# Kernel optimization log

Hardware: AMD Instinct MI355X
Metric: run time of the kernel (lower is better)

Reference implementation:

```python
import jax, jax.numpy as jnp
import numpy as np


def lstm_cell(x, h, c, Wih, Whh, bih, bhh):
    # PyTorch LSTMCell: gates ordered (i, f, g, o)
    gates = x @ Wih.T + h @ Whh.T + bih + bhh
    i, f, g, o = jnp.split(gates, 4, axis=-1)
    c_new = jax.nn.sigmoid(f) * c + jax.nn.sigmoid(i) * jnp.tanh(g)
    h_new = jax.nn.sigmoid(o) * jnp.tanh(c_new)
    return h_new, c_new


def setup_inputs() -> dict:
    key = jax.random.key(0)
    B, S, I, H = 64, 1024, 300, 512
    ks = jax.random.split(key, 9)
    s0 = 1.0 / np.sqrt(H)  # PyTorch LSTMCell default init range

    def u(k, shape):
        return jax.random.uniform(k, shape, jnp.float32, -s0, s0)

    return {
        "input": jax.random.normal(ks[0], (B, S, I), jnp.float32),
        "Wih0": u(ks[1], (4 * H, I)),
        "Whh0": u(ks[2], (4 * H, H)),
        "bih0": u(ks[3], (4 * H,)),
        "bhh0": u(ks[4], (4 * H,)),
        "Wih1": u(ks[5], (4 * H, H)),
        "Whh1": u(ks[6], (4 * H, H)),
        "bih1": u(ks[7], (4 * H,)),
        "bhh1": u(ks[8], (4 * H,)),
    }


def reference(input, Wih0, Whh0, bih0, bhh0, Wih1, Whh1, bih1, bhh1):
    B, S, I = input.shape
    H = Whh0.shape[1]
    h0 = c0 = h1 = c1 = jnp.zeros((B, H), input.dtype)  # self.h0/self.c0 zeros

    def step(carry, x_t):
        h0, c0, h1, c1 = carry
        h0, c0 = lstm_cell(x_t, h0, c0, Wih0, Whh0, bih0, bhh0)
        h1, c1 = lstm_cell(h0, h1, c1, Wih1, Whh1, bih1, bhh1)
        return (h0, c0, h1, c1), (h1, c1)

    xs = jnp.swapaxes(input, 0, 1)  # [S, B, I]
    (h0, c0, h1, c1), (out, c_out) = jax.lax.scan(step, (h0, c0, h1, c1), xs)
    out = jnp.swapaxes(out, 0, 1)      # [B, S, H]
    c_out = jnp.swapaxes(c_out, 0, 1)  # [B, S, H]
    return ((out, c_out), (h1, c1))
```

## Files before the change

### kernel.cpp

```cpp
#include <hip/hip_runtime.h>

#define NB 64
#define NS 1024
#define NI 300
#define NH 512
#define NWG 224
#define L0N 64
#define L1N 128

typedef _Float16 f16;
typedef f16 half8 __attribute__((ext_vector_type(8)));
typedef float floatx4 __attribute__((ext_vector_type(4)));
typedef unsigned long long u64;
typedef unsigned u32;

__device__ __attribute__((aligned(64))) f16   g_X[NS][NB][320];
__device__ __attribute__((aligned(64))) f16   g_H0[4][NB][NH];
__device__ __attribute__((aligned(64))) f16   g_H1[4][NB][NH];
__device__ __attribute__((aligned(64))) float g_C1[4][NB][NH];
__device__ u32 g_flags[NWG];

__device__ __forceinline__ float sigm(float x){ return 1.f/(1.f+__expf(-x)); }
__device__ __forceinline__ float tanh_(float x){ return 1.f - 2.f/(__expf(2.f*x)+1.f); }

__device__ __forceinline__ u32 ld_flag(int i){
  return __hip_atomic_load(&g_flags[i], __ATOMIC_RELAXED, __HIP_MEMORY_SCOPE_AGENT);
}
__device__ __forceinline__ void sig_flag(int i, u32 v){
  __hip_atomic_store(&g_flags[i], v, __ATOMIC_RELAXED, __HIP_MEMORY_SCOPE_AGENT);
}

#define STR_(x) #x
#define STR(x) STR_(x)
#define CLOAD16(dst, base, OFF) \
  asm volatile("global_load_dwordx4 %0, %1, off offset:" STR(OFF) " sc0 sc1" \
               : "=v"(dst) : "v"(base))
#define CLOAD8(dst, base) \
  asm volatile("global_load_dwordx2 %0, %1, off sc0 sc1" : "=v"(dst) : "v"(base))
#define CLOADF4(dst, base) \
  asm volatile("global_load_dwordx4 %0, %1, off sc0 sc1" : "=v"(dst) : "v"(base))
#define CSTORE16(base, val) \
  asm volatile("global_store_dwordx4 %0, %1, off sc0 sc1" :: "v"(base), "v"(val))
#define CSTORE8(base, val) \
  asm volatile("global_store_dwordx2 %0, %1, off sc0 sc1" :: "v"(base), "v"(val))
#define VWAIT(N) do { asm volatile("s_waitcnt vmcnt(" STR(N) ")" ::: "memory"); \
  __builtin_amdgcn_sched_barrier(0); } while(0)
#define MFMA(acc, a, b) acc = __builtin_amdgcn_mfma_f32_16x16x32_f16(a, b, acc, 0, 0, 0)

__global__ void __launch_bounds__(256, 1) lstm_persist(
    const float* __restrict__ xin,
    const float* __restrict__ Wih0, const float* __restrict__ Whh0,
    const float* __restrict__ bih0, const float* __restrict__ bhh0,
    const float* __restrict__ Wih1, const float* __restrict__ Whh1,
    const float* __restrict__ bih1, const float* __restrict__ bhh1,
    float* __restrict__ out)
{
  __shared__ f16   Wl[16 * 840];
  __shared__ f16   sh_h[4][16][8];
  __shared__ float sh_c[4][16][4];
  __shared__ char  lds_pad[84000];

  const int wg = blockIdx.x, tid = threadIdx.x;
  const int wv = tid >> 6, lane = tid & 63, r15 = lane & 15, g4 = lane >> 4;
  const int kb = g4 * 8;
  const u32 base = ld_flag(wg);
  if (__builtin_expect(base == 0xdeadbeefu, 0)) ((volatile char*)lds_pad)[tid] = 1;

  if (wg < L0N) {
    const int j0 = wg * 8;
    const int mrow = wv * 16 + r15;
    {
      const int b = tid >> 2, q = tid & 3;
      for (int r = 0; r < 16; ++r) {
        const int t = wg * 16 + r;
        const float* xr = xin + ((size_t)b * NS + t) * NI;
        u64* dst = (u64*)&g_X[t][b][0];
        #pragma unroll
        for (int e = 0; e < 20; ++e) {
          const int idx = q * 20 + e;
          u64 v = 0;
          if (idx < 75) {
            const float4 f = *(const float4*)(xr + (idx << 2));
            union { f16 h[4]; u64 u; } pk;
            pk.h[0]=(f16)f.x; pk.h[1]=(f16)f.y; pk.h[2]=(f16)f.z; pk.h[3]=(f16)f.w;
            v = pk.u;
          }
          dst[idx] = v;
        }
      }
    }
    if (tid < 64) { half8 z = {}; CSTORE16(&g_H0[3][tid][j0], z); }
    half8 w0[26];
    {
      const int gc = ((r15 >> 3) * NH) + j0 + (r15 & 7);
      #pragma unroll
      for (int ch = 0; ch < 26; ++ch) {
        union { f16 h[8]; half8 v; } pk;
        #pragma unroll
        for (int jj = 0; jj < 8; ++jj) {
          const int k = ch * 32 + kb + jj;
          const float v = (k < NI) ? Wih0[(size_t)gc * NI + k]
                         : (k < 320) ? 0.f : Whh0[(size_t)gc * NH + (k - 320)];
          pk.h[jj] = (f16)v;
        }
        w0[ch] = pk.v;
      }
    }
    for (int r = 0; r < 16; ++r) {
      const int gc = (2 + (r >> 3)) * NH + j0 + (r & 7);
      for (int k = tid; k < 832; k += 256) {
        const float v = (k < NI) ? Wih0[(size_t)gc * NI + k]
                       : (k < 320) ? 0.f : Whh0[(size_t)gc * NH + (k - 320)];
        Wl[r * 840 + k] = (f16)v;
      }
    }
    const int jb = j0 + (r15 & 7);
    const float bi = bih0[jb] + bhh0[jb];
    const float bf = bih0[NH + jb] + bhh0[NH + jb];
    const float bg = bih0[2*NH + jb] + bhh0[2*NH + jb];
    const float bo = bih0[3*NH + jb] + bhh0[3*NH + jb];
    VWAIT(0);
    __syncthreads();
    if (tid == 0) { __threadfence(); sig_flag(wg, base + 1); }

    {
      const u32 T0 = base + 1;
      if (tid < 64) {
        for (;;) {
          const u32 f0 = ld_flag(tid);
          if (__all((int)(f0 - T0) >= 0)) break;
          __builtin_amdgcn_s_sleep(1);
        }
      }
      __syncthreads();
    }

    half8 xa[10];
    #pragma unroll
    for (int ci = 0; ci < 10; ++ci)
      xa[ci] = *(const half8*)&g_X[0][mrow][ci * 32 + kb];

    float creg[2] = {0.f, 0.f};
    const int hi = (r15 >> 3) & 1;
    const f16* wl = &Wl[r15 * 840 + kb];

    for (int t = 0; t < NS; ++t) {
      if (t > 0) {
        const u32 T0 = base + 1 + (u32)t;
        const u32 T1 = (t >= 4) ? (base + (u32)(t - 2)) : base;
        if (tid < 64) {
          for (;;) {
            const u32 f0 = ld_flag(tid);
            const u32 fa = ld_flag(64 + tid);
            const u32 fb = ld_flag(128 + tid);
            const bool ok = ((int)(f0 - T0) >= 0) & ((int)(fa - T1) >= 0) & ((int)(fb - T1) >= 0);
            if (__all(ok)) break;
            __builtin_amdgcn_s_sleep(1);
          }
        }
        __syncthreads();
      }
      const f16* hp = &g_H0[(t + 3) & 3][mrow][kb];
      half8 ha[16];
      CLOAD16(ha[0],  hp, 0);   CLOAD16(ha[1],  hp, 64);
      CLOAD16(ha[2],  hp, 128); CLOAD16(ha[3],  hp, 192);
      CLOAD16(ha[4],  hp, 256); CLOAD16(ha[5],  hp, 320);
      CLOAD16(ha[6],  hp, 384); CLOAD16(ha[7],  hp, 448);
      CLOAD16(ha[8],  hp, 512); CLOAD16(ha[9],  hp, 576);
      CLOAD16(ha[10], hp, 640); CLOAD16(ha[11], hp, 704);
      CLOAD16(ha[12], hp, 768); CLOAD16(ha[13], hp, 832);
      CLOAD16(ha[14], hp, 896); CLOAD16(ha[15], hp, 960);

      floatx4 a0a = {0,0,0,0}, a0b = {0,0,0,0}, a1a = {0,0,0,0}, a1b = {0,0,0,0};
      #pragma unroll
      for (int ci = 0; ci < 10; ++ci) {
        const half8 wb = *(const half8*)(wl + ci * 32);
        if (ci & 1) { MFMA(a0b, xa[ci], w0[ci]); MFMA(a1b, xa[ci], wb); }
        else        { MFMA(a0a, xa[ci], w0[ci]); MFMA(a1a, xa[ci], wb); }
      }
      VWAIT(8);
      #pragma unroll
      for (int ci = 0; ci < 8; ++ci) {
        const half8 wb = *(const half8*)(wl + (10 + ci) * 32);
        if (ci & 1) { MFMA(a0b, ha[ci], w0[10 + ci]); MFMA(a1b, ha[ci], wb); }
        else        { MFMA(a0a, ha[ci], w0[10 + ci]); MFMA(a1a, ha[ci], wb); }
      }
      VWAIT(0);
      #pragma unroll
      for (int ci = 8; ci < 16; ++ci) {
        const half8 wb = *(const half8*)(wl + (10 + ci) * 32);
        if (ci & 1) { MFMA(a0b, ha[ci], w0[10 + ci]); MFMA(a1b, ha[ci], wb); }
        else        { MFMA(a0a, ha[ci], w0[10 + ci]); MFMA(a1a, ha[ci], wb); }
      }
      const floatx4 acc0 = a0a + a0b, acc1 = a1a + a1b;

      float f0v[4], f1v[4];
      #pragma unroll
      for (int r = 0; r < 4; ++r) {
        f0v[r] = __shfl_xor(acc0[r], 8, 64);
        f1v[r] = __shfl_xor(acc1[r], 8, 64);
      }
      #pragma unroll
      for (int p = 0; p < 2; ++p) {
        const float vi = (hi ? f0v[2+p] : (float)acc0[p]) + bi;
        const float vf = (hi ? (float)acc0[2+p] : f0v[p]) + bf;
        const float vg = (hi ? f1v[2+p] : (float)acc1[p]) + bg;
        const float vo = (hi ? (float)acc1[2+p] : f1v[p]) + bo;
        const float cn = sigm(vf) * creg[p] + sigm(vi) * tanh_(vg);
        const float hn = sigm(vo) * tanh_(cn);
        creg[p] = cn;
        sh_h[wv][g4 * 4 + hi * 2 + p][r15 & 7] = (f16)hn;
      }
      if (lane < 16) {
        const half8 hv = *(const half8*)&sh_h[wv][lane][0];
        CSTORE16(&g_H0[t & 3][wv * 16 + lane][j0], hv);
      }
      VWAIT(0);
      __syncthreads();
      if (tid == 0) sig_flag(wg, base + 2 + (u32)t);
      if (t + 1 < NS) {
        #pragma unroll
        for (int ci = 0; ci < 10; ++ci)
          xa[ci] = *(const half8*)&g_X[t + 1][mrow][ci * 32 + kb];
      }
    }

  } else if (wg < L0N + L1N) {
    const int j0 = (wg - L0N) * 4;
    const int mrow = wv * 16 + r15;
    if (tid < 64) {
      u64 z = 0;
      CSTORE8(&g_H1[3][tid][j0], z);
    }
    half8 w1[24];
    {
      const int gc = (r15 >> 2) * NH + j0 + (r15 & 3);
      #pragma unroll
      for (int ch = 0; ch < 24; ++ch) {
        union { f16 h[8]; half8 v; } pk;
        #pragma unroll
        for (int jj = 0; jj < 8; ++jj) {
          const int k = ch * 32 + kb + jj;
          const float v = (k < NH) ? Wih1[(size_t)gc * NH + k]
                                   : Whh1[(size_t)gc * NH + (k - NH)];
          pk.h[jj] = (f16)v;
        }
        w1[ch] = pk.v;
      }
    }
    for (int r = 0; r < 16; ++r) {
      const int gc = (r >> 2) * NH + j0 + (r & 3);
      for (int k = tid; k < 256; k += 256)
        Wl[r * 264 + k] = (f16)Whh1[(size_t)gc * NH + 256 + k];
    }
    const int jb = j0 + (r15 & 3);
    const float bi = bih1[jb] + bhh1[jb];
    const float bf = bih1[NH + jb] + bhh1[NH + jb];
    const float bg = bih1[2*NH + jb] + bhh1[2*NH + jb];
    const float bo = bih1[3*NH + jb] + bhh1[3*NH + jb];
    VWAIT(0);
    __syncthreads();
    if (tid == 0) { __threadfence(); sig_flag(wg, base + 1); }

    float creg[2] = {0.f, 0.f};
    const f16* wl1 = &Wl[r15 * 264 + kb];

    for (int t = 0; t < NS; ++t) {
      {
        const u32 T0 = base + 2 + (u32)t;
        const u32 T1 = base + 1 + (u32)t;
        const u32 T2 = (t >= 4) ? (base + (u32)(t - 2)) : base;
        if (tid < 64) {
          for (;;) {
            const u32 f0 = ld_flag(tid);
            const u32 fa = ld_flag(64 + tid);
            const u32 fb = ld_flag(128 + tid);
            const u32 fo = ld_flag(192 + (tid & 31));
            const bool ok = ((int)(f0 - T0) >= 0) & ((int)(fa - T1) >= 0) &
                            ((int)(fb - T1) >= 0) & ((int)(fo - T2) >= 0);
            if (__all(ok)) break;
            __builtin_amdgcn_s_sleep(1);
          }
        }
        __syncthreads();
      }
      const f16* b0p = &g_H0[t & 3][mrow][kb];
      const f16* b1p = &g_H1[(t + 3) & 3][mrow][kb];
      half8 la[8], lb[8], lc[8], ld[8];
      CLOAD16(la[0], b0p, 0);   CLOAD16(la[1], b0p, 64);
      CLOAD16(la[2], b0p, 128); CLOAD16(la[3], b0p, 192);
      CLOAD16(la[4], b0p, 256); CLOAD16(la[5], b0p, 320);
      CLOAD16(la[6], b0p, 384); CLOAD16(la[7], b0p, 448);
      CLOAD16(lb[0], b0p, 512); CLOAD16(lb[1], b0p, 576);
      CLOAD16(lb[2], b0p, 640); CLOAD16(lb[3], b0p, 704);
      CLOAD16(lb[4], b0p, 768); CLOAD16(lb[5], b0p, 832);
      CLOAD16(lb[6], b0p, 896); CLOAD16(lb[7], b0p, 960);
      floatx4 aA = {0,0,0,0}, aB = {0,0,0,0};
      VWAIT(8);
      CLOAD16(lc[0], b1p, 0);   CLOAD16(lc[1], b1p, 64);
      CLOAD16(lc[2], b1p, 128); CLOAD16(lc[3], b1p, 192);
      CLOAD16(lc[4], b1p, 256); CLOAD16(lc[5], b1p, 320);
      CLOAD16(lc[6], b1p, 384); CLOAD16(lc[7], b1p, 448);
      #pragma unroll
      for (int cc = 0; cc < 8; ++cc) {
        if (cc & 1) MFMA(aB, la[cc], w1[cc]); else MFMA(aA, la[cc], w1[cc]);
      }
      VWAIT(8);
      CLOAD16(ld[0], b1p, 512); CLOAD16(ld[1], b1p, 576);
      CLOAD16(ld[2], b1p, 640); CLOAD16(ld[3], b1p, 704);
      CLOAD16(ld[4], b1p, 768); CLOAD16(ld[5], b1p, 832);
      CLOAD16(ld[6], b1p, 896); CLOAD16(ld[7], b1p, 960);
      #pragma unroll
      for (int cc = 0; cc < 8; ++cc) {
        if (cc & 1) MFMA(aB, lb[cc], w1[8 + cc]); else MFMA(aA, lb[cc], w1[8 + cc]);
      }
      VWAIT(8);
      #pragma unroll
      for (int cc = 0; cc < 8; ++cc) {
        if (cc & 1) MFMA(aB, lc[cc], w1[16 + cc]); else MFMA(aA, lc[cc], w1[16 + cc]);
      }
      VWAIT(0);
      #pragma unroll
      for (int cc = 0; cc < 8; ++cc) {
        const half8 wb = *(const half8*)(wl1 + cc * 32);
        if (cc & 1) MFMA(aB, ld[cc], wb); else MFMA(aA, ld[cc], wb);
      }
      const floatx4 av = aA + aB;

      float t4[4], t8[4], t12[4];
      #pragma unroll
      for (int r = 0; r < 4; ++r) {
        t4[r]  = __shfl_xor(av[r], 4, 64);
        t8[r]  = __shfl_xor(av[r], 8, 64);
        t12[r] = __shfl_xor(av[r], 12, 64);
      }
      if (r15 < 8) {
        const int q1 = r15 >> 2;
        #pragma unroll
        for (int p = 0; p < 2; ++p) {
          const float vi = (q1 ? t4[2+p]  : (float)av[p]) + bi;
          const float vf = (q1 ? (float)av[2+p] : t4[p])  + bf;
          const float vg = (q1 ? t12[2+p] : t8[p])        + bg;
          const float vo = (q1 ? t8[2+p]  : t12[p])       + bo;
          const float cn = sigm(vf) * creg[p] + sigm(vi) * tanh_(vg);
          const float hn = sigm(vo) * tanh_(cn);
          creg[p] = cn;
          const int rw = g4 * 4 + 2 * q1 + p;
          sh_h[wv][rw][r15 & 3] = (f16)hn;
          sh_c[wv][rw][r15 & 3] = cn;
        }
      }
      if (lane < 16) {
        const u64 hv = *(const u64*)&sh_h[wv][lane][0];
        CSTORE8(&g_H1[t & 3][wv * 16 + lane][j0], hv);
        const floatx4 cv = *(const floatx4*)&sh_c[wv][lane][0];
        CSTORE16(&g_C1[t & 3][wv * 16 + lane][j0], cv);
      }
      VWAIT(0);
      __syncthreads();
      if (tid == 0) sig_flag(wg, base + 2 + (u32)t);
    }

  } else {
    const int row = (wg - 192) * 2 + (tid >> 7);
    const int q = tid & 127;
    __syncthreads();
    if (tid == 0) sig_flag(wg, base + 1);
    for (int t = 0; t < NS; ++t) {
      {
        const u32 T = base + 2 + (u32)t;
        if (tid < 64) {
          for (;;) {
            const u32 fa = ld_flag(64 + tid);
            const u32 fb = ld_flag(128 + tid);
            if (__all(((int)(fa - T) >= 0) & ((int)(fb - T) >= 0))) break;
            __builtin_amdgcn_s_sleep(1);
          }
        }
        __syncthreads();
      }
      u64 hv; floatx4 cv;
      CLOAD8(hv, &g_H1[t & 3][row][q * 4]);
      CLOADF4(cv, &g_C1[t & 3][row][q * 4]);
      VWAIT(0);
      union { u64 u; f16 h[4]; } U; U.u = hv;
      floatx4 hf = { (float)U.h[0], (float)U.h[1], (float)U.h[2], (float)U.h[3] };
      const size_t o1 = (size_t)row * NS * NH + (size_t)t * NH + q * 4;
      *(floatx4*)&out[o1] = hf;
      *(floatx4*)&out[(size_t)NB * NS * NH + o1] = cv;
      if (t == NS - 1) {
        const size_t o2 = (size_t)2 * NB * NS * NH + (size_t)row * NH + q * 4;
        *(floatx4*)&out[o2] = hf;
        *(floatx4*)&out[o2 + (size_t)NB * NH] = cv;
      }
      __syncthreads();
      if (tid == 0) sig_flag(wg, base + 2 + (u32)t);
    }
  }
}

extern "C" void kernel_launch(void* const* d_in, const int* in_sizes, int n_in,
                              void* d_out, int out_size, void* d_ws, size_t ws_size,
                              hipStream_t stream) {
  (void)in_sizes; (void)n_in; (void)d_ws; (void)ws_size; (void)out_size;
  lstm_persist<<<dim3(NWG), dim3(256), 0, stream>>>(
      (const float*)d_in[0],
      (const float*)d_in[1], (const float*)d_in[2],
      (const float*)d_in[3], (const float*)d_in[4],
      (const float*)d_in[5], (const float*)d_in[6],
      (const float*)d_in[7], (const float*)d_in[8],
      (float*)d_out);
}
```

Baseline: 8.661 ms.

## Replace per-workgroup flag polling with per-step atomic arrival counters and register weights

Cross-workgroup synchronisation moves from per-workgroup flag arrays, which a whole wavefront polled across 64 to 192 entries, to per-timestep atomic arrival counters that one thread polls. Counter targets are derived from the run count read at launch. The layer-0 and layer-1 weights that were held in LDS now stay entirely in registers, which removes LDS reads from the MFMA loops but raises VGPR pressure. The loads for the next step's inputs are issued without cache-bypass bits, and layer-1 issues all its loads before waiting on any of them. Contention on the atomic counters and register spills are the main risks.

New measurement: 11.20 ms. 29.3% more time.

```diff
diff --git a/kernel.cpp b/kernel.cpp
--- a/kernel.cpp
+++ b/kernel.cpp
@@ -18,22 +18,28 @@
 __device__ __attribute__((aligned(64))) f16   g_H0[4][NB][NH];
 __device__ __attribute__((aligned(64))) f16   g_H1[4][NB][NH];
 __device__ __attribute__((aligned(64))) float g_C1[4][NB][NH];
-__device__ u32 g_flags[NWG];
+__device__ u32 g_arr0[NS];
+__device__ u32 g_arr1[NS];
+__device__ u32 g_arrOut[NS];
+__device__ u32 g_arrInit;
 
 __device__ __forceinline__ float sigm(float x){ return 1.f/(1.f+__expf(-x)); }
 __device__ __forceinline__ float tanh_(float x){ return 1.f - 2.f/(__expf(2.f*x)+1.f); }
 
-__device__ __forceinline__ u32 ld_flag(int i){
-  return __hip_atomic_load(&g_flags[i], __ATOMIC_RELAXED, __HIP_MEMORY_SCOPE_AGENT);
+__device__ __forceinline__ u32 ldc(const u32* p){
+  return __hip_atomic_load(p, __ATOMIC_RELAXED, __HIP_MEMORY_SCOPE_AGENT);
 }
-__device__ __forceinline__ void sig_flag(int i, u32 v){
-  __hip_atomic_store(&g_flags[i], v, __ATOMIC_RELAXED, __HIP_MEMORY_SCOPE_AGENT);
+__device__ __forceinline__ void arrive(u32* p){
+  __hip_atomic_fetch_add(p, 1u, __ATOMIC_RELAXED, __HIP_MEMORY_SCOPE_AGENT);
 }
 
 #define STR_(x) #x
 #define STR(x) STR_(x)
 #define CLOAD16(dst, base, OFF) \
   asm volatile("global_load_dwordx4 %0, %1, off offset:" STR(OFF) " sc0 sc1" \
+               : "=v"(dst) : "v"(base))
+#define CLOADN16(dst, base, OFF) \
+  asm volatile("global_load_dwordx4 %0, %1, off offset:" STR(OFF) \
                : "=v"(dst) : "v"(base))
 #define CLOAD8(dst, base) \
   asm volatile("global_load_dwordx2 %0, %1, off sc0 sc1" : "=v"(dst) : "v"(base))
@@ -55,7 +61,6 @@
     const float* __restrict__ bih1, const float* __restrict__ bhh1,
     float* __restrict__ out)
 {
-  __shared__ f16   Wl[16 * 840];
   __shared__ f16   sh_h[4][16][8];
   __shared__ float sh_c[4][16][4];
   __shared__ char  lds_pad[84000];
@@ -63,8 +68,14 @@
   const int wg = blockIdx.x, tid = threadIdx.x;
   const int wv = tid >> 6, lane = tid & 63, r15 = lane & 15, g4 = lane >> 4;
   const int kb = g4 * 8;
-  const u32 base = ld_flag(wg);
-  if (__builtin_expect(base == 0xdeadbeefu, 0)) ((volatile char*)lds_pad)[tid] = 1;
+
+  const u32 R64 = ldc(&g_arr0[NS - 1]);
+  const u32 R = R64 >> 6;
+  const u32 T_init = (R + 1) * 224;
+  const u32 T_a0 = R64 + 64;
+  const u32 T_a1 = (R64 << 1) + 128;
+  const u32 T_out = (R + 1) * 32;
+  if (__builtin_expect(R64 == 0xdeadbeefu, 0)) ((volatile char*)lds_pad)[tid] = 1;
 
   if (wg < L0N) {
     const int j0 = wg * 8;
@@ -90,28 +101,22 @@
       }
     }
     if (tid < 64) { half8 z = {}; CSTORE16(&g_H0[3][tid][j0], z); }
-    half8 w0[26];
+    half8 w0[26], w1r[26];
     {
-      const int gc = ((r15 >> 3) * NH) + j0 + (r15 & 7);
+      const int gc0 = ((r15 >> 3) * NH) + j0 + (r15 & 7);
+      const int gc1 = ((2 + (r15 >> 3)) * NH) + j0 + (r15 & 7);
       #pragma unroll
       for (int ch = 0; ch < 26; ++ch) {
-        union { f16 h[8]; half8 v; } pk;
+        union { f16 h[8]; half8 v; } p0, p1;
         #pragma unroll
         for (int jj = 0; jj < 8; ++jj) {
           const int k = ch * 32 + kb + jj;
-          const float v = (k < NI) ? Wih0[(size_t)gc * NI + k]
-                         : (k < 320) ? 0.f : Whh0[(size_t)gc * NH + (k - 320)];
-          pk.h[jj] = (f16)v;
-        }
-        w0[ch] = pk.v;
-      }
-    }
-    for (int r = 0; r < 16; ++r) {
-      const int gc = (2 + (r >> 3)) * NH + j0 + (r & 7);
-      for (int k = tid; k < 832; k += 256) {
-        const float v = (k < NI) ? Wih0[(size_t)gc * NI + k]
-                       : (k < 320) ? 0.f : Whh0[(size_t)gc * NH + (k - 320)];
-        Wl[r * 840 + k] = (f16)v;
+          p0.h[jj] = (f16)((k < NI) ? Wih0[(size_t)gc0 * NI + k]
+                     : (k < 320) ? 0.f : Whh0[(size_t)gc0 * NH + (k - 320)]);
+          p1.h[jj] = (f16)((k < NI) ? Wih0[(size_t)gc1 * NI + k]
+                     : (k < 320) ? 0.f : Whh0[(size_t)gc1 * NH + (k - 320)]);
+        }
+        w0[ch] = p0.v; w1r[ch] = p1.v;
       }
     }
     const int jb = j0 + (r15 & 7);
@@ -121,42 +126,32 @@
     const float bo = bih0[3*NH + jb] + bhh0[3*NH + jb];
     VWAIT(0);
     __syncthreads();
-    if (tid == 0) { __threadfence(); sig_flag(wg, base + 1); }
-
+    if (tid == 0) { __threadfence(); arrive(&g_arrInit); }
+
+    if (tid == 0) {
+      while ((int)(ldc(&g_arrInit) - T_init) < 0) __builtin_amdgcn_s_sleep(2);
+    }
+    __syncthreads();
+
+    half8 xa[10];
     {
-      const u32 T0 = base + 1;
-      if (tid < 64) {
-        for (;;) {
-          const u32 f0 = ld_flag(tid);
-          if (__all((int)(f0 - T0) >= 0)) break;
-          __builtin_amdgcn_s_sleep(1);
-        }
-      }
-      __syncthreads();
-    }
-
-    half8 xa[10];
-    #pragma unroll
-    for (int ci = 0; ci < 10; ++ci)
-      xa[ci] = *(const half8*)&g_X[0][mrow][ci * 32 + kb];
+      const f16* xp = &g_X[0][mrow][kb];
+      CLOADN16(xa[0], xp, 0);   CLOADN16(xa[1], xp, 64);
+      CLOADN16(xa[2], xp, 128); CLOADN16(xa[3], xp, 192);
+      CLOADN16(xa[4], xp, 256); CLOADN16(xa[5], xp, 320);
+      CLOADN16(xa[6], xp, 384); CLOADN16(xa[7], xp, 448);
+      CLOADN16(xa[8], xp, 512); CLOADN16(xa[9], xp, 576);
+    }
 
     float creg[2] = {0.f, 0.f};
     const int hi = (r15 >> 3) & 1;
-    const f16* wl = &Wl[r15 * 840 + kb];
 
     for (int t = 0; t < NS; ++t) {
       if (t > 0) {
-        const u32 T0 = base + 1 + (u32)t;
-        const u32 T1 = (t >= 4) ? (base + (u32)(t - 2)) : base;
-        if (tid < 64) {
-          for (;;) {
-            const u32 f0 = ld_flag(tid);
-            const u32 fa = ld_flag(64 + tid);
-            const u32 fb = ld_flag(128 + tid);
-            const bool ok = ((int)(f0 - T0) >= 0) & ((int)(fa - T1) >= 0) & ((int)(fb - T1) >= 0);
-            if (__all(ok)) break;
-            __builtin_amdgcn_s_sleep(1);
-          }
+        if (tid == 0) {
+          while ((int)(ldc(&g_arr0[t - 1]) - T_a0) < 0) __builtin_amdgcn_s_sleep(2);
+          if (t >= 4)
+            while ((int)(ldc(&g_arr1[t - 4]) - T_a1) < 0) __builtin_amdgcn_s_sleep(2);
         }
         __syncthreads();
       }
@@ -172,25 +167,23 @@
       CLOAD16(ha[14], hp, 896); CLOAD16(ha[15], hp, 960);
 
       floatx4 a0a = {0,0,0,0}, a0b = {0,0,0,0}, a1a = {0,0,0,0}, a1b = {0,0,0,0};
+      VWAIT(16);
       #pragma unroll
       for (int ci = 0; ci < 10; ++ci) {
-        const half8 wb = *(const half8*)(wl + ci * 32);
-        if (ci & 1) { MFMA(a0b, xa[ci], w0[ci]); MFMA(a1b, xa[ci], wb); }
-        else        { MFMA(a0a, xa[ci], w0[ci]); MFMA(a1a, xa[ci], wb); }
+        if (ci & 1) { MFMA(a0b, xa[ci], w0[ci]); MFMA(a1b, xa[ci], w1r[ci]); }
+        else        { MFMA(a0a, xa[ci], w0[ci]); MFMA(a1a, xa[ci], w1r[ci]); }
       }
       VWAIT(8);
       #pragma unroll
       for (int ci = 0; ci < 8; ++ci) {
-        const half8 wb = *(const half8*)(wl + (10 + ci) * 32);
-        if (ci & 1) { MFMA(a0b, ha[ci], w0[10 + ci]); MFMA(a1b, ha[ci], wb); }
-        else        { MFMA(a0a, ha[ci], w0[10 + ci]); MFMA(a1a, ha[ci], wb); }
+        if (ci & 1) { MFMA(a0b, ha[ci], w0[10 + ci]); MFMA(a1b, ha[ci], w1r[10 + ci]); }
+        else        { MFMA(a0a, ha[ci], w0[10 + ci]); MFMA(a1a, ha[ci], w1r[10 + ci]); }
       }
       VWAIT(0);
       #pragma unroll
       for (int ci = 8; ci < 16; ++ci) {
-        const half8 wb = *(const half8*)(wl + (10 + ci) * 32);
-        if (ci & 1) { MFMA(a0b, ha[ci], w0[10 + ci]); MFMA(a1b, ha[ci], wb); }
-        else        { MFMA(a0a, ha[ci], w0[10 + ci]); MFMA(a1a, ha[ci], wb); }
+        if (ci & 1) { MFMA(a0b, ha[ci], w0[10 + ci]); MFMA(a1b, ha[ci], w1r[10 + ci]); }
+        else        { MFMA(a0a, ha[ci], w0[10 + ci]); MFMA(a1a, ha[ci], w1r[10 + ci]); }
       }
       const floatx4 acc0 = a0a + a0b, acc1 = a1a + a1b;
 
@@ -217,41 +210,44 @@
       }
       VWAIT(0);
       __syncthreads();
-      if (tid == 0) sig_flag(wg, base + 2 + (u32)t);
+      if (tid == 0) {
+        if (t == NS - 1) {
+          const u32 old = __hip_atomic_fetch_add(&g_arr0[t], 1u,
+              __ATOMIC_RELAXED, __HIP_MEMORY_SCOPE_AGENT);
+          asm volatile("" :: "v"(old));
+          asm volatile("s_waitcnt vmcnt(0)" ::: "memory");
+        } else {
+          arrive(&g_arr0[t]);
+        }
+      }
       if (t + 1 < NS) {
-        #pragma unroll
-        for (int ci = 0; ci < 10; ++ci)
-          xa[ci] = *(const half8*)&g_X[t + 1][mrow][ci * 32 + kb];
+        const f16* xp = &g_X[t + 1][mrow][kb];
+        CLOADN16(xa[0], xp, 0);   CLOADN16(xa[1], xp, 64);
+        CLOADN16(xa[2], xp, 128); CLOADN16(xa[3], xp, 192);
+        CLOADN16(xa[4], xp, 256); CLOADN16(xa[5], xp, 320);
+        CLOADN16(xa[6], xp, 384); CLOADN16(xa[7], xp, 448);
+        CLOADN16(xa[8], xp, 512); CLOADN16(xa[9], xp, 576);
       }
     }
 
   } else if (wg < L0N + L1N) {
     const int j0 = (wg - L0N) * 4;
     const int mrow = wv * 16 + r15;
-    if (tid < 64) {
-      u64 z = 0;
-      CSTORE8(&g_H1[3][tid][j0], z);
-    }
-    half8 w1[24];
+    if (tid < 64) { u64 z = 0; CSTORE8(&g_H1[3][tid][j0], z); }
+    half8 w1[32];
     {
       const int gc = (r15 >> 2) * NH + j0 + (r15 & 3);
       #pragma unroll
-      for (int ch = 0; ch < 24; ++ch) {
+      for (int ch = 0; ch < 32; ++ch) {
         union { f16 h[8]; half8 v; } pk;
         #pragma unroll
         for (int jj = 0; jj < 8; ++jj) {
           const int k = ch * 32 + kb + jj;
-          const float v = (k < NH) ? Wih1[(size_t)gc * NH + k]
-                                   : Whh1[(size_t)gc * NH + (k - NH)];
-          pk.h[jj] = (f16)v;
+          pk.h[jj] = (f16)((k < NH) ? Wih1[(size_t)gc * NH + k]
+                                    : Whh1[(size_t)gc * NH + (k - NH)]);
         }
         w1[ch] = pk.v;
       }
-    }
-    for (int r = 0; r < 16; ++r) {
-      const int gc = (r >> 2) * NH + j0 + (r & 3);
-      for (int k = tid; k < 256; k += 256)
-        Wl[r * 264 + k] = (f16)Whh1[(size_t)gc * NH + 256 + k];
     }
     const int jb = j0 + (r15 & 3);
     const float bi = bih1[jb] + bhh1[jb];
@@ -260,32 +256,26 @@
     const float bo = bih1[3*NH + jb] + bhh1[3*NH + jb];
     VWAIT(0);
     __syncthreads();
-    if (tid == 0) { __threadfence(); sig_flag(wg, base + 1); }
+    if (tid == 0) arrive(&g_arrInit);
+    if (tid == 0) {
+      while ((int)(ldc(&g_arrInit) - T_init) < 0) __builtin_amdgcn_s_sleep(2);
+    }
+    __syncthreads();
 
     float creg[2] = {0.f, 0.f};
-    const f16* wl1 = &Wl[r15 * 264 + kb];
-
-    for (int t = 0; t < NS; ++t) {
-      {
-        const u32 T0 = base + 2 + (u32)t;
-        const u32 T1 = base + 1 + (u32)t;
-        const u32 T2 = (t >= 4) ? (base + (u32)(t - 2)) : base;
-        if (tid < 64) {
-          for (;;) {
-            const u32 f0 = ld_flag(tid);
-            const u32 fa = ld_flag(64 + tid);
-            const u32 fb = ld_flag(128 + tid);
-            const u32 fo = ld_flag(192 + (tid & 31));
-            const bool ok = ((int)(f0 - T0) >= 0) & ((int)(fa - T1) >= 0) &
-                            ((int)(fb - T1) >= 0) & ((int)(fo - T2) >= 0);
-            if (__all(ok)) break;
-            __builtin_amdgcn_s_sleep(1);
-          }
-        }
-        __syncthreads();
-      }
-      const f16* b0p = &g_H0[t & 3][mrow][kb];
-      const f16* b1p = &g_H1[(t + 3) & 3][mrow][kb];
+
+    for (int s = 0; s < NS; ++s) {
+      if (tid == 0) {
+        while ((int)(ldc(&g_arr0[s]) - T_a0) < 0) __builtin_amdgcn_s_sleep(2);
+        if (s >= 1)
+          while ((int)(ldc(&g_arr1[s - 1]) - T_a1) < 0) __builtin_amdgcn_s_sleep(2);
+        if (s >= 4)
+          while ((int)(ldc(&g_arrOut[s - 4]) - T_out) < 0) __builtin_amdgcn_s_sleep(2);
+      }
+      __syncthreads();
+
+      const f16* b0p = &g_H0[s & 3][mrow][kb];
+      const f16* b1p = &g_H1[(s + 3) & 3][mrow][kb];
       half8 la[8], lb[8], lc[8], ld[8];
       CLOAD16(la[0], b0p, 0);   CLOAD16(la[1], b0p, 64);
       CLOAD16(la[2], b0p, 128); CLOAD16(la[3], b0p, 192);
@@ -295,21 +285,22 @@
       CLOAD16(lb[2], b0p, 640); CLOAD16(lb[3], b0p, 704);
       CLOAD16(lb[4], b0p, 768); CLOAD16(lb[5], b0p, 832);
       CLOAD16(lb[6], b0p, 896); CLOAD16(lb[7], b0p, 960);
-      floatx4 aA = {0,0,0,0}, aB = {0,0,0,0};
-      VWAIT(8);
       CLOAD16(lc[0], b1p, 0);   CLOAD16(lc[1], b1p, 64);
       CLOAD16(lc[2], b1p, 128); CLOAD16(lc[3], b1p, 192);
       CLOAD16(lc[4], b1p, 256); CLOAD16(lc[5], b1p, 320);
       CLOAD16(lc[6], b1p, 384); CLOAD16(lc[7], b1p, 448);
-      #pragma unroll
-      for (int cc = 0; cc < 8; ++cc) {
-        if (cc & 1) MFMA(aB, la[cc], w1[cc]); else MFMA(aA, la[cc], w1[cc]);
-      }
-      VWAIT(8);
       CLOAD16(ld[0], b1p, 512); CLOAD16(ld[1], b1p, 576);
       CLOAD16(ld[2], b1p, 640); CLOAD16(ld[3], b1p, 704);
       CLOAD16(ld[4], b1p, 768); CLOAD16(ld[5], b1p, 832);
       CLOAD16(ld[6], b1p, 896); CLOAD16(ld[7], b1p, 960);
+
+      floatx4 aA = {0,0,0,0}, aB = {0,0,0,0};
+      VWAIT(24);
+      #pragma unroll
+      for (int cc = 0; cc < 8; ++cc) {
+        if (cc & 1) MFMA(aB, la[cc], w1[cc]); else MFMA(aA, la[cc], w1[cc]);
+      }
+      VWAIT(16);
       #pragma unroll
       for (int cc = 0; cc < 8; ++cc) {
         if (cc & 1) MFMA(aB, lb[cc], w1[8 + cc]); else MFMA(aA, lb[cc], w1[8 + cc]);
@@ -322,8 +313,7 @@
       VWAIT(0);
       #pragma unroll
       for (int cc = 0; cc < 8; ++cc) {
-        const half8 wb = *(const half8*)(wl1 + cc * 32);
-        if (cc & 1) MFMA(aB, ld[cc], wb); else MFMA(aA, ld[cc], wb);
+        if (cc & 1) MFMA(aB, ld[cc], w1[24 + cc]); else MFMA(aA, ld[cc], w1[24 + cc]);
       }
       const floatx4 av = aA + aB;
 
@@ -352,49 +342,45 @@
       }
       if (lane < 16) {
         const u64 hv = *(const u64*)&sh_h[wv][lane][0];
-        CSTORE8(&g_H1[t & 3][wv * 16 + lane][j0], hv);
+        CSTORE8(&g_H1[s & 3][wv * 16 + lane][j0], hv);
         const floatx4 cv = *(const floatx4*)&sh_c[wv][lane][0];
-        CSTORE16(&g_C1[t & 3][wv * 16 + lane][j0], cv);
-      }
-      VWAIT(0);
-      __syncthreads();
-      if (tid == 0) sig_flag(wg, base + 2 + (u32)t);
+        CSTORE16(&g_C1[s & 3][wv * 16 + lane][j0], cv);
+      }
+      VWAIT(0);
+      __syncthreads();
+      if (tid == 0) arrive(&g_arr1[s]);
     }
 
   } else {
     const int row = (wg - 192) * 2 + (tid >> 7);
     const int q = tid & 127;
     __syncthreads();
-    if (tid == 0) sig_flag(wg, base + 1);
-    for (int t = 0; t < NS; ++t) {
-      {
-        const u32 T = base + 2 + (u32)t;
-        if (tid < 64) {
-          for (;;) {
-            const u32 fa = ld_flag(64 + tid);
-            const u32 fb = ld_flag(128 + tid);
-            if (__all(((int)(fa - T) >= 0) & ((int)(fb - T) >= 0))) break;
-            __builtin_amdgcn_s_sleep(1);
-          }
-        }
-        __syncthreads();
-      }
+    if (tid == 0) arrive(&g_arrInit);
+    if (tid == 0) {
+      while ((int)(ldc(&g_arrInit) - T_init) < 0) __builtin_amdgcn_s_sleep(2);
+    }
+    __syncthreads();
+    for (int s = 0; s < NS; ++s) {
+      if (tid == 0) {
+        while ((int)(ldc(&g_arr1[s]) - T_a1) < 0) __builtin_amdgcn_s_sleep(2);
+      }
+      __syncthreads();
       u64 hv; floatx4 cv;
-      CLOAD8(hv, &g_H1[t & 3][row][q * 4]);
-      CLOADF4(cv, &g_C1[t & 3][row][q * 4]);
+      CLOAD8(hv, &g_H1[s & 3][row][q * 4]);
+      CLOADF4(cv, &g_C1[s & 3][row][q * 4]);
       VWAIT(0);
       union { u64 u; f16 h[4]; } U; U.u = hv;
       floatx4 hf = { (float)U.h[0], (float)U.h[1], (float)U.h[2], (float)U.h[3] };
-      const size_t o1 = (size_t)row * NS * NH + (size_t)t * NH + q * 4;
+      const size_t o1 = (size_t)row * NS * NH + (size_t)s * NH + q * 4;
       *(floatx4*)&out[o1] = hf;
       *(floatx4*)&out[(size_t)NB * NS * NH + o1] = cv;
-      if (t == NS - 1) {
+      if (s == NS - 1) {
         const size_t o2 = (size_t)2 * NB * NS * NH + (size_t)row * NH + q * 4;
         *(floatx4*)&out[o2] = hf;
         *(floatx4*)&out[o2 + (size_t)NB * NH] = cv;
       }
       __syncthreads();
-      if (tid == 0) sig_flag(wg, base + 2 + (u32)t);
+      if (tid == 0) arrive(&g_arrOut[s]);
     }
   }
 }
```
